# Performance work log

Hardware: AMD Instinct MI355X
Metric: run time of the kernel (lower is better)

## Reference

```python
import jax, jax.numpy as jnp
import numpy as np

B, DM, H, M, K = 2, 256, 4, 4096, 16
DIM = DM // H  # per-head feature dim = 64


def _proj(x, W, b):
    # 1x1 Conv2d on channels-first (B, C, M, K): pointwise linear over channels
    return jnp.einsum('oi,bimk->bomk', W, x) + b[None, :, None, None]


def setup_inputs() -> dict:
    rng = jax.random.key(0)
    ks = jax.random.split(rng, 11)
    s = 1.0 / np.sqrt(DM)
    return {
        'query': jax.random.normal(ks[0], (B, DM, M, 1), jnp.float32),
        'key':   jax.random.normal(ks[1], (B, DM, M, K), jnp.float32),
        'value': jax.random.normal(ks[2], (B, DM, M, K), jnp.float32),
        'Wq': jax.random.normal(ks[3], (DM, DM), jnp.float32) * s,
        'bq': jax.random.normal(ks[4], (DM,), jnp.float32) * 0.01,
        'Wk': jax.random.normal(ks[5], (DM, DM), jnp.float32) * s,
        'bk': jax.random.normal(ks[6], (DM,), jnp.float32) * 0.01,
        'Wv': jax.random.normal(ks[7], (DM, DM), jnp.float32) * s,
        'bv': jax.random.normal(ks[8], (DM,), jnp.float32) * 0.01,
        'Wm': jax.random.normal(ks[9], (DM, DM), jnp.float32) * s,
        'bm': jax.random.normal(ks[10], (DM,), jnp.float32) * 0.01,
    }


def reference(query, key, value, Wq, bq, Wk, bk, Wv, bv, Wm, bm):
    # project; torch view(B, dim, heads, -1) on channels-first => channel c -> (d=c//H, h=c%H)
    q = _proj(query, Wq, bq).reshape(B, DIM, H, M)          # (b, d, h, m)
    k = _proj(key,   Wk, bk).reshape(B, DIM, H, M, K)        # (b, d, h, m, k)
    v = _proj(value, Wv, bv).reshape(B, DIM, H, M, K)
    scores = jnp.einsum('bfhm,bfhmk->bhmk', q, k) / np.sqrt(DIM).astype(np.float32)
    prob = jax.nn.softmax(scores, axis=-1)                   # softmax over kn neighbors
    x = jnp.einsum('bhmk,bdhmk->bdhm', prob, v)              # (b, d, h, m)
    out = _proj(x.reshape(B, DM, M, 1), Wm, bm)              # merge 1x1 conv
    prob_sum = jnp.sum(prob, axis=1)                         # (b, m, k)
    return out, prob_sum
```

## Files before the change

### kernel.cpp

```cpp
#include <hip/hip_runtime.h>
#include <stdint.h>

#define DM_ 256
#define H_ 4
#define M_ 4096
#define KN_ 16
#define B_ 2
#define MK_ (M_*KN_)

typedef __attribute__((ext_vector_type(8))) short short8;
typedef __attribute__((ext_vector_type(4))) float f32x4;
typedef __attribute__((ext_vector_type(4))) unsigned short u16x4;

static __device__ __forceinline__ unsigned short f2bf(float x) {
  union { float f; uint32_t u; } v; v.f = x;
  uint32_t u = v.u + (0x7FFFu + ((v.u >> 16) & 1u));
  return (unsigned short)(u >> 16);
}
static __device__ __forceinline__ float bf2f(unsigned short x) {
  union { uint32_t u; float f; } v; v.u = ((uint32_t)x) << 16; return v.f;
}

static __device__ __forceinline__ int swz512(int col, int kbyte) {
  int f = ((col >> 2) & 7) ^ ((col & 1) << 2);
  return (col << 9) + (kbyte ^ (f << 4));
}

__global__ void prep2(const float* __restrict__ Wq, const float* __restrict__ bq,
                      const float* __restrict__ Wk, const float* __restrict__ Wv,
                      const float* __restrict__ bv, const float* __restrict__ Wm,
                      const float* __restrict__ bm,
                      unsigned short* __restrict__ W2T, unsigned short* __restrict__ Wmv,
                      float* __restrict__ qb2, float* __restrict__ btot) {
  int t = blockIdx.x * 512 + threadIdx.x;
  if (t < 262144) {
    int j = t & 7, lane = (t >> 3) & 63, rowblk = (t >> 9) & 63, kstep = t >> 15;
    int row = rowblk * 16 + (lane & 15);
    int k = kstep * 32 + (lane >> 4) * 8 + j;
    int h = row >> 8, c = row & 255;
    float v = 0.f;
#pragma unroll 8
    for (int d = 0; d < 64; ++d) v += Wq[(4 * d + h) * 256 + k] * Wk[(4 * d + h) * 256 + c];
    W2T[t] = f2bf(v);
  } else if (t < 524288) {
    int e = t - 262144;
    int j = e & 7, lane = (e >> 3) & 63, rowblk = (e >> 9) & 15, kstep = e >> 13;
    int o = rowblk * 16 + (lane & 15);
    int kidx = kstep * 32 + (lane >> 4) * 8 + j;
    int c = kidx >> 2, h = kidx & 3;
    float v = 0.f;
#pragma unroll 8
    for (int d = 0; d < 64; ++d) v += Wm[o * 256 + 4 * d + h] * Wv[(4 * d + h) * 256 + c];
    Wmv[e] = f2bf(v);
  } else if (t < 525312) {
    int r = t - 524288; int h = r >> 8, c = r & 255;
    float v = 0.f;
#pragma unroll 8
    for (int d = 0; d < 64; ++d) v += bq[4 * d + h] * Wk[(4 * d + h) * 256 + c];
    qb2[r] = v;
  } else if (t < 525568) {
    int o = t - 525312;
    float v = bm[o];
#pragma unroll 8
    for (int c2 = 0; c2 < 256; ++c2) v += Wm[o * 256 + c2] * bv[c2];
    btot[o] = v;
  }
}

__global__ __launch_bounds__(512)
void qw_gemm(const float* __restrict__ query, const unsigned short* __restrict__ W2T,
             const float* __restrict__ qb2, unsigned short* __restrict__ qWbuf) {
  __shared__ unsigned short Xl[32 * 256];
  const int tid = threadIdx.x;
  const int lane = tid & 63, wid = tid >> 6;
  const int wr = wid >> 1, wc = wid & 1;
  const int mt = blockIdx.x & 127;
  const int rt = (blockIdx.x >> 7) & 3;
  const int b = blockIdx.x >> 9;
  const int m0 = mt * 32;
  const float* Xb = query + (size_t)b * DM_ * M_ + m0;
  const int c4 = 4 * (tid & 7);
  const int ch0 = 4 * (tid >> 3);
  float4 f[4];
#pragma unroll
  for (int i = 0; i < 4; ++i) f[i] = *(const float4*)(Xb + (size_t)(ch0 + i) * M_ + c4);
#pragma unroll
  for (int j = 0; j < 4; ++j) {
    u16x4 u = { f2bf(((const float*)&f[0])[j]), f2bf(((const float*)&f[1])[j]),
                f2bf(((const float*)&f[2])[j]), f2bf(((const float*)&f[3])[j]) };
    *(u16x4*)((char*)Xl + swz512(c4 + j, 2 * ch0)) = u;
  }
  __syncthreads();
  f32x4 acc[4] = {};
  const int bcol = wc * 16 + (lane & 15);
  const int rdk = 16 * (lane >> 4);
  short8 a_cur[4], a_nxt[4];
#pragma unroll
  for (int fi = 0; fi < 4; ++fi)
    a_cur[fi] = *(const short8*)(W2T + (size_t)(((0 * 64 + rt * 16 + wr * 4 + fi) * 64 + lane) * 8));
#pragma unroll
  for (int kgs = 0; kgs < 8; ++kgs) {
    if (kgs < 7) {
#pragma unroll
      for (int fi = 0; fi < 4; ++fi)
        a_nxt[fi] = *(const short8*)(W2T + (size_t)((((kgs + 1) * 64 + rt * 16 + wr * 4 + fi) * 64 + lane) * 8));
    }
    short8 bb = *(const short8*)((const char*)Xl + swz512(bcol, 64 * kgs + rdk));
#pragma unroll
    for (int fi = 0; fi < 4; ++fi)
      acc[fi] = __builtin_amdgcn_mfma_f32_16x16x32_bf16(a_cur[fi], bb, acc[fi], 0, 0, 0);
#pragma unroll
    for (int fi = 0; fi < 4; ++fi) a_cur[fi] = a_nxt[fi];
  }
#pragma unroll
  for (int fi = 0; fi < 4; ++fi) {
#pragma unroll
    for (int r = 0; r < 4; ++r) {
      const int rr = rt * 256 + wr * 64 + fi * 16 + (lane >> 4) * 4 + r;
      qWbuf[(size_t)(b * 1024 + rr) * M_ + m0 + bcol] = f2bf(acc[fi][r] + qb2[rr]);
    }
  }
}

__global__ __launch_bounds__(512, 4)
void attn_stream(const float* __restrict__ key, const float* __restrict__ value,
                 const unsigned short* __restrict__ qWbuf,
                 unsigned short* __restrict__ pvbuf, float* __restrict__ psum) {
  __shared__ float shA[256 * 32];
  __shared__ float scx[8][4][128];
  __shared__ float prob_lds[4][8][16];
  const int tid = threadIdx.x;
  const int lane = tid & 63, w = tid >> 6;
  const int vb = (blockIdx.x & 7) * 128 + (blockIdx.x >> 3);
  const int b = vb >> 9;
  const int m0 = (vb & 511) * 8;
  const int cb = w * 32;
  const int chalf = lane >> 5;
  const int colb = m0 * KN_ + 4 * (lane & 31);
  const int mloc = (lane & 31) >> 2;
  const int kk0 = 4 * (lane & 3);
  const int r0 = tid * 2;
  uint4 qw0 = *(const uint4*)(qWbuf + (size_t)(b * 1024 + r0) * M_ + m0);
  uint4 qw1 = *(const uint4*)(qWbuf + (size_t)(b * 1024 + r0 + 1) * M_ + m0);
  __builtin_amdgcn_sched_barrier(0);
  const float* kp0 = key + (size_t)b * DM_ * MK_ + (size_t)(cb + chalf) * MK_ + colb;
  const float* vp0 = value + (size_t)b * DM_ * MK_ + (size_t)(cb + chalf) * MK_ + colb;
  f32x4 K[16];
#pragma unroll
  for (int i = 0; i < 16; ++i) K[i] = *(const f32x4*)(kp0 + (size_t)(2 * i) * MK_);
  __builtin_amdgcn_sched_barrier(0);
#pragma unroll
  for (int p = 0; p < 2; ++p) {
    const int r = r0 + p;
    const int h = r >> 8, c = r & 255;
    const uint32_t* vu = p ? (const uint32_t*)&qw1 : (const uint32_t*)&qw0;
#pragma unroll
    for (int m = 0; m < 8; ++m)
      shA[c * 32 + m * 4 + h] = bf2f((unsigned short)(vu[m >> 1] >> ((m & 1) * 16)));
  }
  __syncthreads();
  f32x4 s4[4] = {};
  f32x4 V[16];
  const int qb0 = (cb + chalf) * 32 + mloc * 4;
#pragma unroll
  for (int i = 0; i < 16; ++i) {
    V[i] = *(const f32x4*)(vp0 + (size_t)(2 * i) * MK_);
    const f32x4 qv = *(const f32x4*)&shA[qb0 + i * 64];
#pragma unroll
    for (int h = 0; h < 4; ++h) s4[h] += K[i] * qv[h];
    __builtin_amdgcn_sched_barrier(0);
  }
#pragma unroll
  for (int h = 0; h < 4; ++h)
#pragma unroll
    for (int j = 0; j < 4; ++j) {
      float v = s4[h][j];
      v += __shfl_xor(v, 32);
      s4[h][j] = v;
    }
  if (lane < 32) {
#pragma unroll
    for (int h = 0; h < 4; ++h) *(f32x4*)&scx[w][h][4 * lane] = s4[h];
  }
  __syncthreads();
  {
    const int h2 = tid >> 7, col = tid & 127;
    float sc = 0.f;
#pragma unroll
    for (int w2 = 0; w2 < 8; ++w2) sc += scx[w2][h2][col];
    sc *= 0.125f;
    float mx = sc;
#pragma unroll
    for (int d2 = 1; d2 < 16; d2 <<= 1) mx = fmaxf(mx, __shfl_xor(mx, d2));
    const float e = __expf(sc - mx);
    float sm = e;
#pragma unroll
    for (int d2 = 1; d2 < 16; d2 <<= 1) sm += __shfl_xor(sm, d2);
    prob_lds[h2][col >> 4][col & 15] = e / sm;
  }
  __syncthreads();
  if (tid < 128) {
    const int m = tid >> 4, kk = tid & 15;
    psum[(size_t)(b * M_ + m0 + m) * KN_ + kk] =
        prob_lds[0][m][kk] + prob_lds[1][m][kk] + prob_lds[2][m][kk] + prob_lds[3][m][kk];
  }
  f32x4 pr[4];
#pragma unroll
  for (int h = 0; h < 4; ++h) pr[h] = *(const f32x4*)&prob_lds[h][mloc][kk0];
#pragma unroll
  for (int j = 0; j < 16; ++j) {
    const f32x4 vv = V[j];
    float pp[4];
#pragma unroll
    for (int h = 0; h < 4; ++h)
      pp[h] = fmaf(pr[h][0], vv[0], fmaf(pr[h][1], vv[1], fmaf(pr[h][2], vv[2], pr[h][3] * vv[3])));
#pragma unroll
    for (int h = 0; h < 4; ++h) {
      pp[h] += __shfl_xor(pp[h], 1);
      pp[h] += __shfl_xor(pp[h], 2);
    }
    if ((lane & 3) == 0) {
      const int c = cb + 2 * j + chalf;
      f32x4 o = {pp[0], pp[1], pp[2], pp[3]};
      *(f32x4*)&shA[c * 32 + mloc * 4] = o;
    }
  }
  __syncthreads();
  {
    unsigned short o16[16];
#pragma unroll
    for (int ci = 0; ci < 4; ++ci) {
      f32x4 v = *(const f32x4*)&shA[(lane * 4 + ci) * 32 + w * 4];
#pragma unroll
      for (int h = 0; h < 4; ++h) o16[ci * 4 + h] = f2bf(v[h]);
    }
    unsigned short* dst = pvbuf + ((size_t)(b * M_ + m0 + w) * 1024 + lane * 16);
    *(uint4*)dst = *(const uint4*)&o16[0];
    *(uint4*)(dst + 8) = *(const uint4*)&o16[8];
  }
}

__global__ __launch_bounds__(512)
void out_gemm(const unsigned short* __restrict__ pvbuf, const unsigned short* __restrict__ Wmv,
              const float* __restrict__ btot, float* __restrict__ Out) {
  __shared__ unsigned short Xl[2][16 * 256];
  const int tid = threadIdx.x;
  const int lane = tid & 63, wid = tid >> 6;
  const int b = blockIdx.x >> 8;
  const int m0 = (blockIdx.x & 255) * 16;
  const int scol = tid & 15, sq = tid >> 4;
  const int bcol = lane & 15;
  const int rdk = 16 * (lane >> 4);
  f32x4 acc[2] = {};
  for (int kp = 0; kp < 4; ++kp) {
    {
      const unsigned short* src = pvbuf + ((size_t)(b * M_ + m0 + scol) * 1024 + kp * 256 + sq * 8);
      uint4 v0 = *(const uint4*)src;
      *(uint4*)((char*)Xl[kp & 1] + swz512(scol, sq * 16)) = v0;
    }
    __syncthreads();
    short8 a_cur[2], a_nxt[2];
#pragma unroll
    for (int fi = 0; fi < 2; ++fi)
      a_cur[fi] = *(const short8*)(Wmv + (size_t)((((kp * 8) * 16 + wid * 2 + fi) * 64 + lane) * 8));
#pragma unroll
    for (int kgs = 0; kgs < 8; ++kgs) {
      if (kgs < 7) {
#pragma unroll
        for (int fi = 0; fi < 2; ++fi)
          a_nxt[fi] = *(const short8*)(Wmv + (size_t)((((kp * 8 + kgs + 1) * 16 + wid * 2 + fi) * 64 + lane) * 8));
      }
      short8 bb = *(const short8*)((const char*)Xl[kp & 1] + swz512(bcol, 64 * kgs + rdk));
#pragma unroll
      for (int fi = 0; fi < 2; ++fi)
        acc[fi] = __builtin_amdgcn_mfma_f32_16x16x32_bf16(a_cur[fi], bb, acc[fi], 0, 0, 0);
#pragma unroll
      for (int fi = 0; fi < 2; ++fi) a_cur[fi] = a_nxt[fi];
    }
    if (kp < 3) __syncthreads();
  }
#pragma unroll
  for (int fi = 0; fi < 2; ++fi) {
#pragma unroll
    for (int r = 0; r < 4; ++r) {
      const int o = (wid * 2 + fi) * 16 + (lane >> 4) * 4 + r;
      Out[(size_t)(b * DM_ + o) * M_ + m0 + bcol] = acc[fi][r] + btot[o];
    }
  }
}

extern "C" void kernel_launch(void* const* d_in, const int* in_sizes, int n_in,
                              void* d_out, int out_size, void* d_ws, size_t ws_size,
                              hipStream_t stream) {
  const float* query = (const float*)d_in[0];
  const float* key   = (const float*)d_in[1];
  const float* value = (const float*)d_in[2];
  const float* Wq = (const float*)d_in[3];
  const float* bq = (const float*)d_in[4];
  const float* Wk = (const float*)d_in[5];
  const float* bk = (const float*)d_in[6];  (void)bk;
  const float* Wv = (const float*)d_in[7];
  const float* bv = (const float*)d_in[8];
  const float* Wm = (const float*)d_in[9];
  const float* bm = (const float*)d_in[10];
  float* out  = (float*)d_out;
  float* psum = out + (size_t)B_ * DM_ * M_;

  const size_t Wmv_off  = 524288;
  const size_t qb2_off  = 1048576;
  const size_t btot_off = 1052672;
  const size_t qW_off   = 1053696;
  const size_t pv_off   = qW_off + (size_t)B_ * 1024 * M_ * 2;

  unsigned short* W2T   = (unsigned short*)d_ws;
  unsigned short* Wmv   = (unsigned short*)((char*)d_ws + Wmv_off);
  float* qb2            = (float*)((char*)d_ws + qb2_off);
  float* btot           = (float*)((char*)d_ws + btot_off);
  unsigned short* qWbuf = (unsigned short*)((char*)d_ws + qW_off);
  unsigned short* pvbuf = (unsigned short*)((char*)d_ws + pv_off);

  prep2<<<dim3(1027), dim3(512), 0, stream>>>(Wq, bq, Wk, Wv, bv, Wm, bm, W2T, Wmv, qb2, btot);
  qw_gemm<<<dim3(B_ * 4 * 128), dim3(512), 0, stream>>>(query, W2T, qb2, qWbuf);
  attn_stream<<<dim3(B_ * (M_ / 8)), dim3(512), 0, stream>>>(key, value, qWbuf, pvbuf, psum);
  out_gemm<<<dim3(B_ * 256), dim3(512), 0, stream>>>(pvbuf, Wmv, btot, out);
}
```

Before: 117.3 us.

## Restructure attention stream kernel with smaller tiles, inline-asm loads and staged waits

The attention kernel now processes 4 queries per block instead of 8, doubling the grid, and issues all key and value loads up front via inline global_load_dwordx4. Per-step s_waitcnt counters let score and PV compute overlap the remaining in-flight loads. The qW buffer is written by qw_gemm in a per-tile interleaved layout, so one coalesced load and a bf16 LDS tile replace the old fp32 scatter. PV results are packed to bf16 in LDS before a single vector store. This aims to raise memory-level parallelism on the key/value stream, at the cost of fragile hand-counted vmcnt values and a lower occupancy hint.

```diff
diff --git a/kernel.cpp b/kernel.cpp
--- a/kernel.cpp
+++ b/kernel.cpp
@@ -17,8 +17,8 @@
   uint32_t u = v.u + (0x7FFFu + ((v.u >> 16) & 1u));
   return (unsigned short)(u >> 16);
 }
-static __device__ __forceinline__ float bf2f(unsigned short x) {
-  union { uint32_t u; float f; } v; v.u = ((uint32_t)x) << 16; return v.f;
+static __device__ __forceinline__ float u2f(uint32_t u) {
+  union { uint32_t u; float f; } v; v.u = u; return v.f;
 }
 
 static __device__ __forceinline__ int swz512(int col, int kbyte) {
@@ -74,9 +74,10 @@
   const int tid = threadIdx.x;
   const int lane = tid & 63, wid = tid >> 6;
   const int wr = wid >> 1, wc = wid & 1;
-  const int mt = blockIdx.x & 127;
-  const int rt = (blockIdx.x >> 7) & 3;
-  const int b = blockIdx.x >> 9;
+  const int vb = (blockIdx.x & 7) * 128 + (blockIdx.x >> 3);
+  const int rt = vb & 3;
+  const int mt = (vb >> 2) & 127;
+  const int b = vb >> 9;
   const int m0 = mt * 32;
   const float* Xb = query + (size_t)b * DM_ * M_ + m0;
   const int c4 = 4 * (tid & 7);
@@ -97,7 +98,7 @@
   short8 a_cur[4], a_nxt[4];
 #pragma unroll
   for (int fi = 0; fi < 4; ++fi)
-    a_cur[fi] = *(const short8*)(W2T + (size_t)(((0 * 64 + rt * 16 + wr * 4 + fi) * 64 + lane) * 8));
+    a_cur[fi] = *(const short8*)(W2T + (size_t)(((rt * 16 + wr * 4 + fi) * 64 + lane) * 8));
 #pragma unroll
   for (int kgs = 0; kgs < 8; ++kgs) {
     if (kgs < 7) {
@@ -112,79 +113,88 @@
 #pragma unroll
     for (int fi = 0; fi < 4; ++fi) a_cur[fi] = a_nxt[fi];
   }
+  const int m = m0 + bcol;
+  const int mt4 = m >> 2, mq = m & 3;
 #pragma unroll
   for (int fi = 0; fi < 4; ++fi) {
 #pragma unroll
     for (int r = 0; r < 4; ++r) {
-      const int rr = rt * 256 + wr * 64 + fi * 16 + (lane >> 4) * 4 + r;
-      qWbuf[(size_t)(b * 1024 + rr) * M_ + m0 + bcol] = f2bf(acc[fi][r] + qb2[rr]);
-    }
-  }
-}
-
-__global__ __launch_bounds__(512, 4)
+      const int c = wr * 64 + fi * 16 + (lane >> 4) * 4 + r;
+      const int rr = rt * 256 + c;
+      qWbuf[((size_t)(b * 1024 + mt4)) * 4096 + c * 16 + mq * 4 + rt] =
+          f2bf(acc[fi][r] + qb2[rr]);
+    }
+  }
+}
+
+__global__ __launch_bounds__(512, 3)
 void attn_stream(const float* __restrict__ key, const float* __restrict__ value,
                  const unsigned short* __restrict__ qWbuf,
                  unsigned short* __restrict__ pvbuf, float* __restrict__ psum) {
-  __shared__ float shA[256 * 32];
-  __shared__ float scx[8][4][128];
-  __shared__ float prob_lds[4][8][16];
+  __shared__ unsigned short qwtile[4096];
+  __shared__ float scx[8][4][64];
+  __shared__ float prob_lds[4][4][16];
   const int tid = threadIdx.x;
   const int lane = tid & 63, w = tid >> 6;
-  const int vb = (blockIdx.x & 7) * 128 + (blockIdx.x >> 3);
-  const int b = vb >> 9;
-  const int m0 = (vb & 511) * 8;
+  const int vb = (blockIdx.x & 7) * 256 + (blockIdx.x >> 3);
+  const int b = vb >> 10;
+  const int m0 = (vb & 1023) * 4;
+  const int g = lane >> 4, l15 = lane & 15;
+  const int mq = l15 & 3;
+  const int kq = 4 * (l15 >> 2);
+  const int colw = mq * 16 + kq;
   const int cb = w * 32;
-  const int chalf = lane >> 5;
-  const int colb = m0 * KN_ + 4 * (lane & 31);
-  const int mloc = (lane & 31) >> 2;
-  const int kk0 = 4 * (lane & 3);
-  const int r0 = tid * 2;
-  uint4 qw0 = *(const uint4*)(qWbuf + (size_t)(b * 1024 + r0) * M_ + m0);
-  uint4 qw1 = *(const uint4*)(qWbuf + (size_t)(b * 1024 + r0 + 1) * M_ + m0);
+  const float* kb  = key   + (size_t)b * DM_ * MK_;
+  const float* vbp = value + (size_t)b * DM_ * MK_;
+  const unsigned short* qwsrc = qWbuf + ((size_t)(b * 1024 + (m0 >> 2))) * 4096;
+  const uint32_t qwoff = (uint32_t)tid * 16u;
+  const uint32_t kvo = ((uint32_t)(cb + g) * (uint32_t)MK_ +
+                        (uint32_t)(m0 * KN_) + (uint32_t)colw) * 4u;
+  uint4 qwv;
+  f32x4 K[8], V[8];
+  asm volatile("global_load_dwordx4 %0, %1, %2" : "=v"(qwv) : "v"(qwoff), "s"(qwsrc));
+#define GK(i) asm volatile("global_load_dwordx4 %0, %1, %2" : "=v"(K[i]) : "v"(kvo + (i)*1048576u), "s"(kb))
+#define GV(i) asm volatile("global_load_dwordx4 %0, %1, %2" : "=v"(V[i]) : "v"(kvo + (i)*1048576u), "s"(vbp))
+  GK(0); GK(1); GK(2); GK(3); GK(4); GK(5); GK(6); GK(7);
+  GV(0); GV(1); GV(2); GV(3); GV(4); GV(5); GV(6); GV(7);
+#undef GK
+#undef GV
+  asm volatile("s_waitcnt vmcnt(16)" ::: "memory");
   __builtin_amdgcn_sched_barrier(0);
-  const float* kp0 = key + (size_t)b * DM_ * MK_ + (size_t)(cb + chalf) * MK_ + colb;
-  const float* vp0 = value + (size_t)b * DM_ * MK_ + (size_t)(cb + chalf) * MK_ + colb;
-  f32x4 K[16];
-#pragma unroll
-  for (int i = 0; i < 16; ++i) K[i] = *(const f32x4*)(kp0 + (size_t)(2 * i) * MK_);
-  __builtin_amdgcn_sched_barrier(0);
-#pragma unroll
-  for (int p = 0; p < 2; ++p) {
-    const int r = r0 + p;
-    const int h = r >> 8, c = r & 255;
-    const uint32_t* vu = p ? (const uint32_t*)&qw1 : (const uint32_t*)&qw0;
-#pragma unroll
-    for (int m = 0; m < 8; ++m)
-      shA[c * 32 + m * 4 + h] = bf2f((unsigned short)(vu[m >> 1] >> ((m & 1) * 16)));
-  }
-  __syncthreads();
+  *(uint4*)(qwtile + tid * 8) = qwv;
+  __syncthreads();
+  uint2 qvr[8];
+#pragma unroll
+  for (int i = 0; i < 8; ++i)
+    qvr[i] = *(const uint2*)(qwtile + ((cb + 4 * i + g) * 16 + mq * 4));
   f32x4 s4[4] = {};
-  f32x4 V[16];
-  const int qb0 = (cb + chalf) * 32 + mloc * 4;
-#pragma unroll
-  for (int i = 0; i < 16; ++i) {
-    V[i] = *(const f32x4*)(vp0 + (size_t)(2 * i) * MK_);
-    const f32x4 qv = *(const f32x4*)&shA[qb0 + i * 64];
-#pragma unroll
-    for (int h = 0; h < 4; ++h) s4[h] += K[i] * qv[h];
-    __builtin_amdgcn_sched_barrier(0);
-  }
-#pragma unroll
-  for (int h = 0; h < 4; ++h)
+#define KSTEP(i, n) do { \
+    asm volatile("s_waitcnt vmcnt(" #n ")" ::: "memory"); \
+    __builtin_amdgcn_sched_barrier(0); \
+    const uint32_t qx = qvr[i].x, qy = qvr[i].y; \
+    s4[0] += K[i] * u2f(qx << 16); s4[1] += K[i] * u2f(qx & 0xFFFF0000u); \
+    s4[2] += K[i] * u2f(qy << 16); s4[3] += K[i] * u2f(qy & 0xFFFF0000u); \
+  } while (0)
+  KSTEP(0, 15); KSTEP(1, 14); KSTEP(2, 13); KSTEP(3, 12);
+  KSTEP(4, 11); KSTEP(5, 10); KSTEP(6, 9);  KSTEP(7, 8);
+#undef KSTEP
+#pragma unroll
+  for (int h = 0; h < 4; ++h) {
 #pragma unroll
     for (int j = 0; j < 4; ++j) {
       float v = s4[h][j];
+      v += __shfl_xor(v, 16);
       v += __shfl_xor(v, 32);
       s4[h][j] = v;
     }
-  if (lane < 32) {
-#pragma unroll
-    for (int h = 0; h < 4; ++h) *(f32x4*)&scx[w][h][4 * lane] = s4[h];
-  }
-  __syncthreads();
-  {
-    const int h2 = tid >> 7, col = tid & 127;
+  }
+  if (g == 0) {
+#pragma unroll
+    for (int h = 0; h < 4; ++h) *(f32x4*)&scx[w][h][colw] = s4[h];
+  }
+  __syncthreads();
+  if (tid < 256) {
+    const int h2 = tid >> 6, col = tid & 63;
     float sc = 0.f;
 #pragma unroll
     for (int w2 = 0; w2 < 8; ++w2) sc += scx[w2][h2][col];
@@ -199,44 +209,39 @@
     prob_lds[h2][col >> 4][col & 15] = e / sm;
   }
   __syncthreads();
-  if (tid < 128) {
+  if (tid < 64) {
     const int m = tid >> 4, kk = tid & 15;
-    psum[(size_t)(b * M_ + m0 + m) * KN_ + kk] =
+    psum[((size_t)b * M_ + m0 + m) * KN_ + kk] =
         prob_lds[0][m][kk] + prob_lds[1][m][kk] + prob_lds[2][m][kk] + prob_lds[3][m][kk];
   }
   f32x4 pr[4];
 #pragma unroll
-  for (int h = 0; h < 4; ++h) pr[h] = *(const f32x4*)&prob_lds[h][mloc][kk0];
-#pragma unroll
-  for (int j = 0; j < 16; ++j) {
-    const f32x4 vv = V[j];
-    float pp[4];
-#pragma unroll
-    for (int h = 0; h < 4; ++h)
-      pp[h] = fmaf(pr[h][0], vv[0], fmaf(pr[h][1], vv[1], fmaf(pr[h][2], vv[2], pr[h][3] * vv[3])));
-#pragma unroll
-    for (int h = 0; h < 4; ++h) {
-      pp[h] += __shfl_xor(pp[h], 1);
-      pp[h] += __shfl_xor(pp[h], 2);
-    }
-    if ((lane & 3) == 0) {
-      const int c = cb + 2 * j + chalf;
-      f32x4 o = {pp[0], pp[1], pp[2], pp[3]};
-      *(f32x4*)&shA[c * 32 + mloc * 4] = o;
-    }
-  }
+  for (int h = 0; h < 4; ++h) pr[h] = *(const f32x4*)&prob_lds[h][mq][kq];
+#define PSTEP(j, n) do { \
+    asm volatile("s_waitcnt vmcnt(" #n ")" ::: "memory"); \
+    __builtin_amdgcn_sched_barrier(0); \
+    float p0 = pr[0][0]*V[j][0] + pr[0][1]*V[j][1] + pr[0][2]*V[j][2] + pr[0][3]*V[j][3]; \
+    float p1 = pr[1][0]*V[j][0] + pr[1][1]*V[j][1] + pr[1][2]*V[j][2] + pr[1][3]*V[j][3]; \
+    float p2 = pr[2][0]*V[j][0] + pr[2][1]*V[j][1] + pr[2][2]*V[j][2] + pr[2][3]*V[j][3]; \
+    float p3 = pr[3][0]*V[j][0] + pr[3][1]*V[j][1] + pr[3][2]*V[j][2] + pr[3][3]*V[j][3]; \
+    p0 += __shfl_xor(p0, 4); p0 += __shfl_xor(p0, 8); \
+    p1 += __shfl_xor(p1, 4); p1 += __shfl_xor(p1, 8); \
+    p2 += __shfl_xor(p2, 4); p2 += __shfl_xor(p2, 8); \
+    p3 += __shfl_xor(p3, 4); p3 += __shfl_xor(p3, 8); \
+    if (l15 < 4) { \
+      uint2 o; \
+      o.x = (uint32_t)f2bf(p0) | ((uint32_t)f2bf(p1) << 16); \
+      o.y = (uint32_t)f2bf(p2) | ((uint32_t)f2bf(p3) << 16); \
+      *(uint2*)(qwtile + (mq * 1024 + (cb + 4 * (j) + g) * 4)) = o; \
+    } \
+  } while (0)
+  PSTEP(0, 7); PSTEP(1, 6); PSTEP(2, 5); PSTEP(3, 4);
+  PSTEP(4, 3); PSTEP(5, 2); PSTEP(6, 1); PSTEP(7, 0);
+#undef PSTEP
   __syncthreads();
   {
-    unsigned short o16[16];
-#pragma unroll
-    for (int ci = 0; ci < 4; ++ci) {
-      f32x4 v = *(const f32x4*)&shA[(lane * 4 + ci) * 32 + w * 4];
-#pragma unroll
-      for (int h = 0; h < 4; ++h) o16[ci * 4 + h] = f2bf(v[h]);
-    }
-    unsigned short* dst = pvbuf + ((size_t)(b * M_ + m0 + w) * 1024 + lane * 16);
-    *(uint4*)dst = *(const uint4*)&o16[0];
-    *(uint4*)(dst + 8) = *(const uint4*)&o16[8];
+    uint4 ov = *(const uint4*)(qwtile + tid * 8);
+    *(uint4*)(pvbuf + (((size_t)b * M_ + m0 + (tid >> 7)) * 1024 + (tid & 127) * 8)) = ov;
   }
 }
 
@@ -321,6 +326,6 @@
 
   prep2<<<dim3(1027), dim3(512), 0, stream>>>(Wq, bq, Wk, Wv, bv, Wm, bm, W2T, Wmv, qb2, btot);
   qw_gemm<<<dim3(B_ * 4 * 128), dim3(512), 0, stream>>>(query, W2T, qb2, qWbuf);
-  attn_stream<<<dim3(B_ * (M_ / 8)), dim3(512), 0, stream>>>(key, value, qWbuf, pvbuf, psum);
+  attn_stream<<<dim3(B_ * (M_ / 4)), dim3(512), 0, stream>>>(key, value, qWbuf, pvbuf, psum);
   out_gemm<<<dim3(B_ * 256), dim3(512), 0, stream>>>(pvbuf, Wmv, btot, out);
 }
```

Result: slower. 130.6 us (+11.3%).

## Split fused attention into score, softmax and PV kernels with asm-pipelined loads

Applied to the files above, without the earlier changes.

Replaces the single attention kernel with three kernels. The first computes partial scores per channel group, the second reduces them and applies softmax while writing bf16 probabilities and psum, and the third applies the probabilities to value. The key and value streams are read with inline-asm global loads kept twelve deep, each followed by an explicit vmcnt wait, to hold many requests in flight. The cost is extra intermediate traffic through workspace buffers (partial scores and probabilities), two more launches, and workspace aliasing: prob reuses qWbuf and pvbuf reuses psbuf.

```diff
diff --git a/kernel.cpp b/kernel.cpp
--- a/kernel.cpp
+++ b/kernel.cpp
@@ -17,8 +17,8 @@
   uint32_t u = v.u + (0x7FFFu + ((v.u >> 16) & 1u));
   return (unsigned short)(u >> 16);
 }
-static __device__ __forceinline__ float bf2f(unsigned short x) {
-  union { uint32_t u; float f; } v; v.u = ((uint32_t)x) << 16; return v.f;
+static __device__ __forceinline__ float u2f(uint32_t u) {
+  union { uint32_t u; float f; } v; v.u = u; return v.f;
 }
 
 static __device__ __forceinline__ int swz512(int col, int kbyte) {
@@ -97,7 +97,7 @@
   short8 a_cur[4], a_nxt[4];
 #pragma unroll
   for (int fi = 0; fi < 4; ++fi)
-    a_cur[fi] = *(const short8*)(W2T + (size_t)(((0 * 64 + rt * 16 + wr * 4 + fi) * 64 + lane) * 8));
+    a_cur[fi] = *(const short8*)(W2T + (size_t)(((rt * 16 + wr * 4 + fi) * 64 + lane) * 8));
 #pragma unroll
   for (int kgs = 0; kgs < 8; ++kgs) {
     if (kgs < 7) {
@@ -123,120 +123,177 @@
 }
 
 __global__ __launch_bounds__(512, 4)
-void attn_stream(const float* __restrict__ key, const float* __restrict__ value,
-                 const unsigned short* __restrict__ qWbuf,
-                 unsigned short* __restrict__ pvbuf, float* __restrict__ psum) {
-  __shared__ float shA[256 * 32];
-  __shared__ float scx[8][4][128];
-  __shared__ float prob_lds[4][8][16];
+void score_part(const float* __restrict__ key, const unsigned short* __restrict__ qW,
+                float* __restrict__ psbuf) {
+  __shared__ unsigned short qsl[32 * 128 * 4];
   const int tid = threadIdx.x;
-  const int lane = tid & 63, w = tid >> 6;
-  const int vb = (blockIdx.x & 7) * 128 + (blockIdx.x >> 3);
-  const int b = vb >> 9;
-  const int m0 = (vb & 511) * 8;
-  const int cb = w * 32;
-  const int chalf = lane >> 5;
-  const int colb = m0 * KN_ + 4 * (lane & 31);
-  const int mloc = (lane & 31) >> 2;
-  const int kk0 = 4 * (lane & 3);
-  const int r0 = tid * 2;
-  uint4 qw0 = *(const uint4*)(qWbuf + (size_t)(b * 1024 + r0) * M_ + m0);
-  uint4 qw1 = *(const uint4*)(qWbuf + (size_t)(b * 1024 + r0 + 1) * M_ + m0);
+  const int bid = blockIdx.x;
+  const int cg = bid & 7, msb = (bid >> 3) & 31, b = bid >> 8;
+  const int m0 = msb * 128, C0 = cg * 32;
+  {
+    const int row = tid >> 2, part = tid & 3;
+    const int h = row >> 5, c = row & 31;
+    const unsigned short* src = qW + (size_t)(b * 1024 + h * 256 + C0 + c) * M_ + m0 + part * 32;
+#pragma unroll
+    for (int p = 0; p < 4; ++p) {
+      uint4 v = *(const uint4*)(src + p * 8);
+      const uint32_t* vu = (const uint32_t*)&v;
+#pragma unroll
+      for (int e = 0; e < 4; ++e) {
+        const int mm = part * 32 + p * 8 + e * 2;
+        qsl[(c * 128 + mm) * 4 + h]     = (unsigned short)(vu[e] & 0xffffu);
+        qsl[(c * 128 + mm + 1) * 4 + h] = (unsigned short)(vu[e] >> 16);
+      }
+    }
+  }
+  __syncthreads();
+  const int mq = tid >> 2;
+  const int kq = (tid & 3) * 4;
+  const float* kp = key + (size_t)(b * 256 + C0) * 65536 + (size_t)m0 * 16;
+  const uint32_t voff = (uint32_t)((mq * 16 + kq) * 4);
+  f32x4 K[12];
+#define GK(s, cc) asm volatile("global_load_dwordx4 %0, %1, %2" : "=v"(K[s]) : "v"(voff), "s"(kp + (size_t)(cc) * 65536))
+  GK(0,0); GK(1,1); GK(2,2); GK(3,3); GK(4,4); GK(5,5);
+  GK(6,6); GK(7,7); GK(8,8); GK(9,9); GK(10,10); GK(11,11);
+  f32x4 ps0 = {}, ps1 = {}, ps2 = {}, ps3 = {};
+#define AIT(c, n) { \
+    asm volatile("s_waitcnt vmcnt(" #n ")" ::: "memory"); \
+    __builtin_amdgcn_sched_barrier(0); \
+    uint2 qv = *(const uint2*)&qsl[((c) * 128 + mq) * 4]; \
+    float h0 = u2f(qv.x << 16), h1 = u2f(qv.x & 0xffff0000u); \
+    float h2 = u2f(qv.y << 16), h3 = u2f(qv.y & 0xffff0000u); \
+    ps0 += K[(c) % 12] * h0; ps1 += K[(c) % 12] * h1; \
+    ps2 += K[(c) % 12] * h2; ps3 += K[(c) % 12] * h3; \
+    if ((c) < 20) { GK((c) % 12, (c) + 12); } \
+  }
+  AIT(0,11) AIT(1,11) AIT(2,11) AIT(3,11) AIT(4,11) AIT(5,11) AIT(6,11) AIT(7,11)
+  AIT(8,11) AIT(9,11) AIT(10,11) AIT(11,11) AIT(12,11) AIT(13,11) AIT(14,11) AIT(15,11)
+  AIT(16,11) AIT(17,11) AIT(18,11) AIT(19,11) AIT(20,11) AIT(21,10) AIT(22,9) AIT(23,8)
+  AIT(24,7) AIT(25,6) AIT(26,5) AIT(27,4) AIT(28,3) AIT(29,2) AIT(30,1) AIT(31,0)
+#undef AIT
+#undef GK
+  float* pso = psbuf + ((size_t)((b * 8 + cg) * 4096 + m0 + mq) * 16 + kq) * 4;
+#pragma unroll
+  for (int j = 0; j < 4; ++j) {
+    f32x4 o = {ps0[j], ps1[j], ps2[j], ps3[j]};
+    *(f32x4*)(pso + j * 4) = o;
+  }
+}
+
+__global__ __launch_bounds__(512)
+void softmax_k(const float* __restrict__ psbuf, unsigned short* __restrict__ prob,
+               float* __restrict__ psum) {
+  const int tid = threadIdx.x, bid = blockIdx.x;
+  const int b = bid >> 7;
+  const int m = (bid & 127) * 32 + (tid >> 4);
+  const int cp = (tid >> 2) & 3, h = tid & 3;
+  float s[16];
+#pragma unroll
+  for (int kk = 0; kk < 16; ++kk) s[kk] = 0.f;
+#pragma unroll
+  for (int gi = 0; gi < 2; ++gi) {
+    const int g = cp * 2 + gi;
+    const float* pp = psbuf + (size_t)((b * 8 + g) * 4096 + m) * 64 + h;
+#pragma unroll
+    for (int kk = 0; kk < 16; ++kk) s[kk] += pp[kk * 4];
+  }
+#pragma unroll
+  for (int kk = 0; kk < 16; ++kk) {
+    s[kk] += __shfl_xor(s[kk], 4);
+    s[kk] += __shfl_xor(s[kk], 8);
+    s[kk] *= 0.125f;
+  }
+  float mx = s[0];
+#pragma unroll
+  for (int kk = 1; kk < 16; ++kk) mx = fmaxf(mx, s[kk]);
+  float sm = 0.f;
+#pragma unroll
+  for (int kk = 0; kk < 16; ++kk) { s[kk] = __expf(s[kk] - mx); sm += s[kk]; }
+  const float inv = 1.f / sm;
+#pragma unroll
+  for (int kk = 0; kk < 16; ++kk) s[kk] *= inv;
+  if (cp == 0) {
+    unsigned short o16[16];
+#pragma unroll
+    for (int kk = 0; kk < 16; ++kk) o16[kk] = f2bf(s[kk]);
+    unsigned short* dst = prob + ((size_t)(b * 4096 + m) * 4 + h) * 16;
+    *(uint4*)dst = *(const uint4*)&o16[0];
+    *(uint4*)(dst + 8) = *(const uint4*)&o16[8];
+  }
+#pragma unroll
+  for (int kk = 0; kk < 16; ++kk) {
+    s[kk] += __shfl_xor(s[kk], 1);
+    s[kk] += __shfl_xor(s[kk], 2);
+  }
+  if (cp == 0 && h == 0) {
+    float* dst = psum + ((size_t)b * M_ + m) * 16;
+#pragma unroll
+    for (int j = 0; j < 4; ++j) {
+      f32x4 o = {s[j * 4], s[j * 4 + 1], s[j * 4 + 2], s[j * 4 + 3]};
+      *(f32x4*)(dst + j * 4) = o;
+    }
+  }
+}
+
+__global__ __launch_bounds__(512, 4)
+void pv_part(const float* __restrict__ value, const unsigned short* __restrict__ prob,
+             unsigned short* __restrict__ pvbuf) {
+  __shared__ unsigned short pvt[128 * 132];
+  const int tid = threadIdx.x;
+  const int bid = blockIdx.x;
+  const int cg = bid & 7, msb = (bid >> 3) & 31, b = bid >> 8;
+  const int m0 = msb * 128, C0 = cg * 32;
+  const int mq = tid >> 2, kq4 = tid & 3;
+  const unsigned short* pb = prob + (size_t)(b * 4096 + m0) * 64;
+  const uint32_t pvo = (uint32_t)(mq * 128 + kq4 * 8);
+  uint2 pw0, pw1, pw2, pw3;
+  asm volatile("global_load_dwordx2 %0, %1, %2"           : "=v"(pw0) : "v"(pvo), "s"(pb));
+  asm volatile("global_load_dwordx2 %0, %1, %2 offset:32" : "=v"(pw1) : "v"(pvo), "s"(pb));
+  asm volatile("global_load_dwordx2 %0, %1, %2 offset:64" : "=v"(pw2) : "v"(pvo), "s"(pb));
+  asm volatile("global_load_dwordx2 %0, %1, %2 offset:96" : "=v"(pw3) : "v"(pvo), "s"(pb));
+  const float* vp = value + (size_t)(b * 256 + C0) * 65536 + (size_t)m0 * 16;
+  const uint32_t voff = (uint32_t)((mq * 16 + kq4 * 4) * 4);
+  f32x4 V[12];
+#define GV(s, cc) asm volatile("global_load_dwordx4 %0, %1, %2" : "=v"(V[s]) : "v"(voff), "s"(vp + (size_t)(cc) * 65536))
+  GV(0,0); GV(1,1); GV(2,2); GV(3,3); GV(4,4); GV(5,5);
+  GV(6,6); GV(7,7); GV(8,8); GV(9,9); GV(10,10); GV(11,11);
+  asm volatile("s_waitcnt vmcnt(12)" ::: "memory");
   __builtin_amdgcn_sched_barrier(0);
-  const float* kp0 = key + (size_t)b * DM_ * MK_ + (size_t)(cb + chalf) * MK_ + colb;
-  const float* vp0 = value + (size_t)b * DM_ * MK_ + (size_t)(cb + chalf) * MK_ + colb;
-  f32x4 K[16];
-#pragma unroll
-  for (int i = 0; i < 16; ++i) K[i] = *(const f32x4*)(kp0 + (size_t)(2 * i) * MK_);
-  __builtin_amdgcn_sched_barrier(0);
-#pragma unroll
-  for (int p = 0; p < 2; ++p) {
-    const int r = r0 + p;
-    const int h = r >> 8, c = r & 255;
-    const uint32_t* vu = p ? (const uint32_t*)&qw1 : (const uint32_t*)&qw0;
-#pragma unroll
-    for (int m = 0; m < 8; ++m)
-      shA[c * 32 + m * 4 + h] = bf2f((unsigned short)(vu[m >> 1] >> ((m & 1) * 16)));
-  }
-  __syncthreads();
-  f32x4 s4[4] = {};
-  f32x4 V[16];
-  const int qb0 = (cb + chalf) * 32 + mloc * 4;
-#pragma unroll
-  for (int i = 0; i < 16; ++i) {
-    V[i] = *(const f32x4*)(vp0 + (size_t)(2 * i) * MK_);
-    const f32x4 qv = *(const f32x4*)&shA[qb0 + i * 64];
-#pragma unroll
-    for (int h = 0; h < 4; ++h) s4[h] += K[i] * qv[h];
-    __builtin_amdgcn_sched_barrier(0);
-  }
-#pragma unroll
-  for (int h = 0; h < 4; ++h)
-#pragma unroll
-    for (int j = 0; j < 4; ++j) {
-      float v = s4[h][j];
-      v += __shfl_xor(v, 32);
-      s4[h][j] = v;
-    }
-  if (lane < 32) {
-#pragma unroll
-    for (int h = 0; h < 4; ++h) *(f32x4*)&scx[w][h][4 * lane] = s4[h];
-  }
+  f32x4 pr0 = {u2f(pw0.x << 16), u2f(pw0.x & 0xffff0000u), u2f(pw0.y << 16), u2f(pw0.y & 0xffff0000u)};
+  f32x4 pr1 = {u2f(pw1.x << 16), u2f(pw1.x & 0xffff0000u), u2f(pw1.y << 16), u2f(pw1.y & 0xffff0000u)};
+  f32x4 pr2 = {u2f(pw2.x << 16), u2f(pw2.x & 0xffff0000u), u2f(pw2.y << 16), u2f(pw2.y & 0xffff0000u)};
+  f32x4 pr3 = {u2f(pw3.x << 16), u2f(pw3.x & 0xffff0000u), u2f(pw3.y << 16), u2f(pw3.y & 0xffff0000u)};
+  const bool k0 = (kq4 == 0), k1 = (kq4 == 1), k2 = (kq4 == 2);
+#define CIT(c, n) { \
+    asm volatile("s_waitcnt vmcnt(" #n ")" ::: "memory"); \
+    __builtin_amdgcn_sched_barrier(0); \
+    f32x4 vv = V[(c) % 12]; \
+    float p0 = vv[0]*pr0[0] + vv[1]*pr0[1] + vv[2]*pr0[2] + vv[3]*pr0[3]; \
+    float p1 = vv[0]*pr1[0] + vv[1]*pr1[1] + vv[2]*pr1[2] + vv[3]*pr1[3]; \
+    float p2 = vv[0]*pr2[0] + vv[1]*pr2[1] + vv[2]*pr2[2] + vv[3]*pr2[3]; \
+    float p3 = vv[0]*pr3[0] + vv[1]*pr3[1] + vv[2]*pr3[2] + vv[3]*pr3[3]; \
+    p0 += __shfl_xor(p0, 1); p0 += __shfl_xor(p0, 2); \
+    p1 += __shfl_xor(p1, 1); p1 += __shfl_xor(p1, 2); \
+    p2 += __shfl_xor(p2, 1); p2 += __shfl_xor(p2, 2); \
+    p3 += __shfl_xor(p3, 1); p3 += __shfl_xor(p3, 2); \
+    float psel = k0 ? p0 : (k1 ? p1 : (k2 ? p2 : p3)); \
+    pvt[mq * 132 + (c) * 4 + kq4] = f2bf(psel); \
+    if ((c) < 20) { GV((c) % 12, (c) + 12); } \
+  }
+  CIT(0,11) CIT(1,11) CIT(2,11) CIT(3,11) CIT(4,11) CIT(5,11) CIT(6,11) CIT(7,11)
+  CIT(8,11) CIT(9,11) CIT(10,11) CIT(11,11) CIT(12,11) CIT(13,11) CIT(14,11) CIT(15,11)
+  CIT(16,11) CIT(17,11) CIT(18,11) CIT(19,11) CIT(20,11) CIT(21,10) CIT(22,9) CIT(23,8)
+  CIT(24,7) CIT(25,6) CIT(26,5) CIT(27,4) CIT(28,3) CIT(29,2) CIT(30,1) CIT(31,0)
+#undef CIT
+#undef GV
   __syncthreads();
   {
-    const int h2 = tid >> 7, col = tid & 127;
-    float sc = 0.f;
-#pragma unroll
-    for (int w2 = 0; w2 < 8; ++w2) sc += scx[w2][h2][col];
-    sc *= 0.125f;
-    float mx = sc;
-#pragma unroll
-    for (int d2 = 1; d2 < 16; d2 <<= 1) mx = fmaxf(mx, __shfl_xor(mx, d2));
-    const float e = __expf(sc - mx);
-    float sm = e;
-#pragma unroll
-    for (int d2 = 1; d2 < 16; d2 <<= 1) sm += __shfl_xor(sm, d2);
-    prob_lds[h2][col >> 4][col & 15] = e / sm;
-  }
-  __syncthreads();
-  if (tid < 128) {
-    const int m = tid >> 4, kk = tid & 15;
-    psum[(size_t)(b * M_ + m0 + m) * KN_ + kk] =
-        prob_lds[0][m][kk] + prob_lds[1][m][kk] + prob_lds[2][m][kk] + prob_lds[3][m][kk];
-  }
-  f32x4 pr[4];
-#pragma unroll
-  for (int h = 0; h < 4; ++h) pr[h] = *(const f32x4*)&prob_lds[h][mloc][kk0];
-#pragma unroll
-  for (int j = 0; j < 16; ++j) {
-    const f32x4 vv = V[j];
-    float pp[4];
-#pragma unroll
-    for (int h = 0; h < 4; ++h)
-      pp[h] = fmaf(pr[h][0], vv[0], fmaf(pr[h][1], vv[1], fmaf(pr[h][2], vv[2], pr[h][3] * vv[3])));
-#pragma unroll
-    for (int h = 0; h < 4; ++h) {
-      pp[h] += __shfl_xor(pp[h], 1);
-      pp[h] += __shfl_xor(pp[h], 2);
-    }
-    if ((lane & 3) == 0) {
-      const int c = cb + 2 * j + chalf;
-      f32x4 o = {pp[0], pp[1], pp[2], pp[3]};
-      *(f32x4*)&shA[c * 32 + mloc * 4] = o;
-    }
-  }
-  __syncthreads();
-  {
-    unsigned short o16[16];
-#pragma unroll
-    for (int ci = 0; ci < 4; ++ci) {
-      f32x4 v = *(const f32x4*)&shA[(lane * 4 + ci) * 32 + w * 4];
-#pragma unroll
-      for (int h = 0; h < 4; ++h) o16[ci * 4 + h] = f2bf(v[h]);
-    }
-    unsigned short* dst = pvbuf + ((size_t)(b * M_ + m0 + w) * 1024 + lane * 16);
-    *(uint4*)dst = *(const uint4*)&o16[0];
-    *(uint4*)(dst + 8) = *(const uint4*)&o16[8];
+    const int row = tid >> 2, part = tid & 3;
+    unsigned short* dst = pvbuf + (size_t)(b * 4096 + m0 + row) * 1024 + C0 * 4 + part * 32;
+    const unsigned short* srcl = &pvt[row * 132 + part * 32];
+#pragma unroll
+    for (int j = 0; j < 4; ++j)
+      *(uint4*)(dst + j * 8) = *(const uint4*)(srcl + j * 8);
   }
 }
 
@@ -310,17 +367,21 @@
   const size_t qb2_off  = 1048576;
   const size_t btot_off = 1052672;
   const size_t qW_off   = 1053696;
-  const size_t pv_off   = qW_off + (size_t)B_ * 1024 * M_ * 2;
+  const size_t ps_off   = qW_off + (size_t)B_ * 1024 * M_ * 2;
 
   unsigned short* W2T   = (unsigned short*)d_ws;
   unsigned short* Wmv   = (unsigned short*)((char*)d_ws + Wmv_off);
   float* qb2            = (float*)((char*)d_ws + qb2_off);
   float* btot           = (float*)((char*)d_ws + btot_off);
   unsigned short* qWbuf = (unsigned short*)((char*)d_ws + qW_off);
-  unsigned short* pvbuf = (unsigned short*)((char*)d_ws + pv_off);
+  unsigned short* prob  = qWbuf;
+  float* psbuf          = (float*)((char*)d_ws + ps_off);
+  unsigned short* pvbuf = (unsigned short*)((char*)d_ws + ps_off);
 
   prep2<<<dim3(1027), dim3(512), 0, stream>>>(Wq, bq, Wk, Wv, bv, Wm, bm, W2T, Wmv, qb2, btot);
   qw_gemm<<<dim3(B_ * 4 * 128), dim3(512), 0, stream>>>(query, W2T, qb2, qWbuf);
-  attn_stream<<<dim3(B_ * (M_ / 8)), dim3(512), 0, stream>>>(key, value, qWbuf, pvbuf, psum);
+  score_part<<<dim3(512), dim3(512), 0, stream>>>(key, qWbuf, psbuf);
+  softmax_k<<<dim3(256), dim3(512), 0, stream>>>(psbuf, prob, psum);
+  pv_part<<<dim3(512), dim3(512), 0, stream>>>(value, prob, pvbuf);
   out_gemm<<<dim3(B_ * 256), dim3(512), 0, stream>>>(pvbuf, Wmv, btot, out);
 }
```

After: 407.9 us. 248% more time.

## Fuse attention streaming with output projection GEMM in one kernel

Applied to the files above, without the earlier changes.

Merges the attention-streaming kernel and the output GEMM into a single kernel. Each block now handles 16 query points instead of 8 and keeps the bf16 PV result in shared memory, so the pvbuf round trip through global memory and one launch are gone. Key/value access is reorganised so each thread reads float4 along the neighbor axis with a per-row channel split, and reductions use shuffles in place of LDS staging. The trade-offs are half as many blocks (512), which lowers parallelism for the memory-bound key/value stream, and an unpipelined MFMA loop that loads weights directly from global memory.

```diff
diff --git a/kernel.cpp b/kernel.cpp
--- a/kernel.cpp
+++ b/kernel.cpp
@@ -17,8 +17,8 @@
   uint32_t u = v.u + (0x7FFFu + ((v.u >> 16) & 1u));
   return (unsigned short)(u >> 16);
 }
-static __device__ __forceinline__ float bf2f(unsigned short x) {
-  union { uint32_t u; float f; } v; v.u = ((uint32_t)x) << 16; return v.f;
+static __device__ __forceinline__ float u2f(uint32_t u) {
+  union { uint32_t u; float f; } v; v.u = u; return v.f;
 }
 
 static __device__ __forceinline__ int swz512(int col, int kbyte) {
@@ -97,7 +97,7 @@
   short8 a_cur[4], a_nxt[4];
 #pragma unroll
   for (int fi = 0; fi < 4; ++fi)
-    a_cur[fi] = *(const short8*)(W2T + (size_t)(((0 * 64 + rt * 16 + wr * 4 + fi) * 64 + lane) * 8));
+    a_cur[fi] = *(const short8*)(W2T + (size_t)(((rt * 16 + wr * 4 + fi) * 64 + lane) * 8));
 #pragma unroll
   for (int kgs = 0; kgs < 8; ++kgs) {
     if (kgs < 7) {
@@ -123,168 +123,125 @@
 }
 
 __global__ __launch_bounds__(512, 4)
-void attn_stream(const float* __restrict__ key, const float* __restrict__ value,
-                 const unsigned short* __restrict__ qWbuf,
-                 unsigned short* __restrict__ pvbuf, float* __restrict__ psum) {
-  __shared__ float shA[256 * 32];
-  __shared__ float scx[8][4][128];
-  __shared__ float prob_lds[4][8][16];
+void fused_attn(const float* __restrict__ key, const float* __restrict__ value,
+                const unsigned short* __restrict__ qW, const unsigned short* __restrict__ Wmv,
+                const float* __restrict__ btot, float* __restrict__ out,
+                float* __restrict__ psum) {
+  __shared__ unsigned short sh[16384];
   const int tid = threadIdx.x;
-  const int lane = tid & 63, w = tid >> 6;
-  const int vb = (blockIdx.x & 7) * 128 + (blockIdx.x >> 3);
-  const int b = vb >> 9;
-  const int m0 = (vb & 511) * 8;
-  const int cb = w * 32;
-  const int chalf = lane >> 5;
-  const int colb = m0 * KN_ + 4 * (lane & 31);
-  const int mloc = (lane & 31) >> 2;
-  const int kk0 = 4 * (lane & 3);
-  const int r0 = tid * 2;
-  uint4 qw0 = *(const uint4*)(qWbuf + (size_t)(b * 1024 + r0) * M_ + m0);
-  uint4 qw1 = *(const uint4*)(qWbuf + (size_t)(b * 1024 + r0 + 1) * M_ + m0);
-  __builtin_amdgcn_sched_barrier(0);
-  const float* kp0 = key + (size_t)b * DM_ * MK_ + (size_t)(cb + chalf) * MK_ + colb;
-  const float* vp0 = value + (size_t)b * DM_ * MK_ + (size_t)(cb + chalf) * MK_ + colb;
-  f32x4 K[16];
-#pragma unroll
-  for (int i = 0; i < 16; ++i) K[i] = *(const f32x4*)(kp0 + (size_t)(2 * i) * MK_);
-  __builtin_amdgcn_sched_barrier(0);
-#pragma unroll
-  for (int p = 0; p < 2; ++p) {
-    const int r = r0 + p;
-    const int h = r >> 8, c = r & 255;
-    const uint32_t* vu = p ? (const uint32_t*)&qw1 : (const uint32_t*)&qw0;
-#pragma unroll
-    for (int m = 0; m < 8; ++m)
-      shA[c * 32 + m * 4 + h] = bf2f((unsigned short)(vu[m >> 1] >> ((m & 1) * 16)));
-  }
-  __syncthreads();
-  f32x4 s4[4] = {};
-  f32x4 V[16];
-  const int qb0 = (cb + chalf) * 32 + mloc * 4;
-#pragma unroll
-  for (int i = 0; i < 16; ++i) {
-    V[i] = *(const f32x4*)(vp0 + (size_t)(2 * i) * MK_);
-    const f32x4 qv = *(const f32x4*)&shA[qb0 + i * 64];
-#pragma unroll
-    for (int h = 0; h < 4; ++h) s4[h] += K[i] * qv[h];
-    __builtin_amdgcn_sched_barrier(0);
-  }
-#pragma unroll
-  for (int h = 0; h < 4; ++h)
-#pragma unroll
-    for (int j = 0; j < 4; ++j) {
-      float v = s4[h][j];
-      v += __shfl_xor(v, 32);
-      s4[h][j] = v;
-    }
-  if (lane < 32) {
-#pragma unroll
-    for (int h = 0; h < 4; ++h) *(f32x4*)&scx[w][h][4 * lane] = s4[h];
-  }
-  __syncthreads();
+  const int lane = tid & 63;
+  const int vb = (blockIdx.x & 7) * 64 + (blockIdx.x >> 3);
+  const int b = vb >> 8;
+  const int mt = vb & 255;
+  const int m0 = mt * 16;
   {
-    const int h2 = tid >> 7, col = tid & 127;
-    float sc = 0.f;
-#pragma unroll
-    for (int w2 = 0; w2 < 8; ++w2) sc += scx[w2][h2][col];
-    sc *= 0.125f;
-    float mx = sc;
-#pragma unroll
-    for (int d2 = 1; d2 < 16; d2 <<= 1) mx = fmaxf(mx, __shfl_xor(mx, d2));
-    const float e = __expf(sc - mx);
-    float sm = e;
-#pragma unroll
-    for (int d2 = 1; d2 < 16; d2 <<= 1) sm += __shfl_xor(sm, d2);
-    prob_lds[h2][col >> 4][col & 15] = e / sm;
-  }
-  __syncthreads();
-  if (tid < 128) {
-    const int m = tid >> 4, kk = tid & 15;
-    psum[(size_t)(b * M_ + m0 + m) * KN_ + kk] =
-        prob_lds[0][m][kk] + prob_lds[1][m][kk] + prob_lds[2][m][kk] + prob_lds[3][m][kk];
-  }
-  f32x4 pr[4];
-#pragma unroll
-  for (int h = 0; h < 4; ++h) pr[h] = *(const f32x4*)&prob_lds[h][mloc][kk0];
-#pragma unroll
-  for (int j = 0; j < 16; ++j) {
-    const f32x4 vv = V[j];
-    float pp[4];
-#pragma unroll
-    for (int h = 0; h < 4; ++h)
-      pp[h] = fmaf(pr[h][0], vv[0], fmaf(pr[h][1], vv[1], fmaf(pr[h][2], vv[2], pr[h][3] * vv[3])));
-#pragma unroll
-    for (int h = 0; h < 4; ++h) {
-      pp[h] += __shfl_xor(pp[h], 1);
-      pp[h] += __shfl_xor(pp[h], 2);
-    }
-    if ((lane & 3) == 0) {
-      const int c = cb + 2 * j + chalf;
-      f32x4 o = {pp[0], pp[1], pp[2], pp[3]};
-      *(f32x4*)&shA[c * 32 + mloc * 4] = o;
+    const int c = tid & 255, hh = (tid >> 8) << 1;
+    uint4 rv[2][2];
+#pragma unroll
+    for (int h2 = 0; h2 < 2; ++h2) {
+      const unsigned short* src = qW + ((size_t)(b * 1024 + (hh + h2) * 256 + c)) * M_ + m0;
+      rv[h2][0] = *(const uint4*)(src);
+      rv[h2][1] = *(const uint4*)(src + 8);
+    }
+    const unsigned short* rs = (const unsigned short*)rv;
+#pragma unroll
+    for (int q = 0; q < 16; ++q) {
+      const int slot = (q + c) & 15;
+      const uint32_t o = (uint32_t)rs[q] | ((uint32_t)rs[16 + q] << 16);
+      *(uint32_t*)&sh[c * 64 + slot * 4 + hh] = o;
+    }
+  }
+  __syncthreads();
+  const int mq = tid >> 5;
+  const int cs = (tid >> 2) & 7;
+  const int kq = tid & 3;
+  const float* kp = key + (size_t)(b * 256) * 65536 + (size_t)m0 * 16;
+  const float* vp = value + (size_t)(b * 256) * 65536 + (size_t)m0 * 16;
+  const int moff = mq * 16 + kq * 4;
+  f32x4 ps0 = {}, ps1 = {}, ps2 = {}, ps3 = {};
+#pragma unroll 2
+  for (int cc = 0; cc < 8; ++cc) {
+#pragma unroll
+    for (int i = 0; i < 4; ++i) {
+      const int c = cc * 32 + cs * 4 + i;
+      const f32x4 kv = *(const f32x4*)(kp + (size_t)c * 65536 + moff);
+      const int slot = (mq + c) & 15;
+      const uint2 qv = *(const uint2*)&sh[c * 64 + slot * 4];
+      ps0 += kv * u2f(qv.x << 16);
+      ps1 += kv * u2f(qv.x & 0xffff0000u);
+      ps2 += kv * u2f(qv.y << 16);
+      ps3 += kv * u2f(qv.y & 0xffff0000u);
+    }
+  }
+#pragma unroll
+  for (int j = 0; j < 4; ++j) {
+    ps0[j] += __shfl_xor(ps0[j], 4); ps0[j] += __shfl_xor(ps0[j], 8); ps0[j] += __shfl_xor(ps0[j], 16);
+    ps1[j] += __shfl_xor(ps1[j], 4); ps1[j] += __shfl_xor(ps1[j], 8); ps1[j] += __shfl_xor(ps1[j], 16);
+    ps2[j] += __shfl_xor(ps2[j], 4); ps2[j] += __shfl_xor(ps2[j], 8); ps2[j] += __shfl_xor(ps2[j], 16);
+    ps3[j] += __shfl_xor(ps3[j], 4); ps3[j] += __shfl_xor(ps3[j], 8); ps3[j] += __shfl_xor(ps3[j], 16);
+  }
+  f32x4 pr0, pr1, pr2, pr3;
+#define SOFT(ps, pr) { \
+    f32x4 s = ps * 0.125f; \
+    float mx = fmaxf(fmaxf(s[0], s[1]), fmaxf(s[2], s[3])); \
+    mx = fmaxf(mx, __shfl_xor(mx, 1)); mx = fmaxf(mx, __shfl_xor(mx, 2)); \
+    f32x4 e; \
+    e[0] = __expf(s[0] - mx); e[1] = __expf(s[1] - mx); \
+    e[2] = __expf(s[2] - mx); e[3] = __expf(s[3] - mx); \
+    float sm = e[0] + e[1] + e[2] + e[3]; \
+    sm += __shfl_xor(sm, 1); sm += __shfl_xor(sm, 2); \
+    const float inv = 1.f / sm; \
+    pr[0] = e[0] * inv; pr[1] = e[1] * inv; pr[2] = e[2] * inv; pr[3] = e[3] * inv; \
+  }
+  SOFT(ps0, pr0) SOFT(ps1, pr1) SOFT(ps2, pr2) SOFT(ps3, pr3)
+#undef SOFT
+  if (cs == 0) {
+    f32x4 pp = pr0 + pr1 + pr2 + pr3;
+    *(f32x4*)(psum + ((size_t)b * M_ + m0 + mq) * KN_ + kq * 4) = pp;
+  }
+  __syncthreads();
+#pragma unroll 2
+  for (int cc = 0; cc < 8; ++cc) {
+#pragma unroll
+    for (int i = 0; i < 4; ++i) {
+      const int c = cc * 32 + cs * 4 + i;
+      const f32x4 vv = *(const f32x4*)(vp + (size_t)c * 65536 + moff);
+      float p0 = vv[0] * pr0[0] + vv[1] * pr0[1] + vv[2] * pr0[2] + vv[3] * pr0[3];
+      float p1 = vv[0] * pr1[0] + vv[1] * pr1[1] + vv[2] * pr1[2] + vv[3] * pr1[3];
+      float p2 = vv[0] * pr2[0] + vv[1] * pr2[1] + vv[2] * pr2[2] + vv[3] * pr2[3];
+      float p3 = vv[0] * pr3[0] + vv[1] * pr3[1] + vv[2] * pr3[2] + vv[3] * pr3[3];
+      p0 += __shfl_xor(p0, 1); p0 += __shfl_xor(p0, 2);
+      p1 += __shfl_xor(p1, 1); p1 += __shfl_xor(p1, 2);
+      p2 += __shfl_xor(p2, 1); p2 += __shfl_xor(p2, 2);
+      p3 += __shfl_xor(p3, 1); p3 += __shfl_xor(p3, 2);
+      if (kq == 0) {
+        uint2 o;
+        o.x = (uint32_t)f2bf(p0) | ((uint32_t)f2bf(p1) << 16);
+        o.y = (uint32_t)f2bf(p2) | ((uint32_t)f2bf(p3) << 16);
+        *(uint2*)((char*)sh + ((mq * 2048 + c * 8) ^ ((mq & 7) << 4))) = o;
+      }
     }
   }
   __syncthreads();
   {
-    unsigned short o16[16];
-#pragma unroll
-    for (int ci = 0; ci < 4; ++ci) {
-      f32x4 v = *(const f32x4*)&shA[(lane * 4 + ci) * 32 + w * 4];
-#pragma unroll
-      for (int h = 0; h < 4; ++h) o16[ci * 4 + h] = f2bf(v[h]);
-    }
-    unsigned short* dst = pvbuf + ((size_t)(b * M_ + m0 + w) * 1024 + lane * 16);
-    *(uint4*)dst = *(const uint4*)&o16[0];
-    *(uint4*)(dst + 8) = *(const uint4*)&o16[8];
-  }
-}
-
-__global__ __launch_bounds__(512)
-void out_gemm(const unsigned short* __restrict__ pvbuf, const unsigned short* __restrict__ Wmv,
-              const float* __restrict__ btot, float* __restrict__ Out) {
-  __shared__ unsigned short Xl[2][16 * 256];
-  const int tid = threadIdx.x;
-  const int lane = tid & 63, wid = tid >> 6;
-  const int b = blockIdx.x >> 8;
-  const int m0 = (blockIdx.x & 255) * 16;
-  const int scol = tid & 15, sq = tid >> 4;
-  const int bcol = lane & 15;
-  const int rdk = 16 * (lane >> 4);
-  f32x4 acc[2] = {};
-  for (int kp = 0; kp < 4; ++kp) {
-    {
-      const unsigned short* src = pvbuf + ((size_t)(b * M_ + m0 + scol) * 1024 + kp * 256 + sq * 8);
-      uint4 v0 = *(const uint4*)src;
-      *(uint4*)((char*)Xl[kp & 1] + swz512(scol, sq * 16)) = v0;
-    }
-    __syncthreads();
-    short8 a_cur[2], a_nxt[2];
-#pragma unroll
-    for (int fi = 0; fi < 2; ++fi)
-      a_cur[fi] = *(const short8*)(Wmv + (size_t)((((kp * 8) * 16 + wid * 2 + fi) * 64 + lane) * 8));
-#pragma unroll
-    for (int kgs = 0; kgs < 8; ++kgs) {
-      if (kgs < 7) {
-#pragma unroll
-        for (int fi = 0; fi < 2; ++fi)
-          a_nxt[fi] = *(const short8*)(Wmv + (size_t)((((kp * 8 + kgs + 1) * 16 + wid * 2 + fi) * 64 + lane) * 8));
-      }
-      short8 bb = *(const short8*)((const char*)Xl[kp & 1] + swz512(bcol, 64 * kgs + rdk));
-#pragma unroll
-      for (int fi = 0; fi < 2; ++fi)
-        acc[fi] = __builtin_amdgcn_mfma_f32_16x16x32_bf16(a_cur[fi], bb, acc[fi], 0, 0, 0);
-#pragma unroll
-      for (int fi = 0; fi < 2; ++fi) a_cur[fi] = a_nxt[fi];
-    }
-    if (kp < 3) __syncthreads();
-  }
-#pragma unroll
-  for (int fi = 0; fi < 2; ++fi) {
+    const int wid = tid >> 6;
+    const int bcol = lane & 15;
+    const int kgrp = lane >> 4;
+    f32x4 acc0 = {}, acc1 = {};
+    for (int kgs = 0; kgs < 32; ++kgs) {
+      const int byte = (bcol * 2048 + kgs * 64 + kgrp * 16) ^ ((bcol & 7) << 4);
+      const short8 bb = *(const short8*)((const char*)sh + byte);
+      const short8 a0 = *(const short8*)(Wmv + (size_t)(((kgs * 16 + wid * 2 + 0) * 64 + lane) * 8));
+      const short8 a1 = *(const short8*)(Wmv + (size_t)(((kgs * 16 + wid * 2 + 1) * 64 + lane) * 8));
+      acc0 = __builtin_amdgcn_mfma_f32_16x16x32_bf16(a0, bb, acc0, 0, 0, 0);
+      acc1 = __builtin_amdgcn_mfma_f32_16x16x32_bf16(a1, bb, acc1, 0, 0, 0);
+    }
 #pragma unroll
     for (int r = 0; r < 4; ++r) {
-      const int o = (wid * 2 + fi) * 16 + (lane >> 4) * 4 + r;
-      Out[(size_t)(b * DM_ + o) * M_ + m0 + bcol] = acc[fi][r] + btot[o];
+      const int o0 = (wid * 2 + 0) * 16 + kgrp * 4 + r;
+      const int o1 = (wid * 2 + 1) * 16 + kgrp * 4 + r;
+      out[((size_t)(b * DM_ + o0)) * M_ + m0 + bcol] = acc0[r] + btot[o0];
+      out[((size_t)(b * DM_ + o1)) * M_ + m0 + bcol] = acc1[r] + btot[o1];
     }
   }
 }
@@ -310,17 +267,14 @@
   const size_t qb2_off  = 1048576;
   const size_t btot_off = 1052672;
   const size_t qW_off   = 1053696;
-  const size_t pv_off   = qW_off + (size_t)B_ * 1024 * M_ * 2;
 
   unsigned short* W2T   = (unsigned short*)d_ws;
   unsigned short* Wmv   = (unsigned short*)((char*)d_ws + Wmv_off);
   float* qb2            = (float*)((char*)d_ws + qb2_off);
   float* btot           = (float*)((char*)d_ws + btot_off);
   unsigned short* qWbuf = (unsigned short*)((char*)d_ws + qW_off);
-  unsigned short* pvbuf = (unsigned short*)((char*)d_ws + pv_off);
 
   prep2<<<dim3(1027), dim3(512), 0, stream>>>(Wq, bq, Wk, Wv, bv, Wm, bm, W2T, Wmv, qb2, btot);
   qw_gemm<<<dim3(B_ * 4 * 128), dim3(512), 0, stream>>>(query, W2T, qb2, qWbuf);
-  attn_stream<<<dim3(B_ * (M_ / 8)), dim3(512), 0, stream>>>(key, value, qWbuf, pvbuf, psum);
-  out_gemm<<<dim3(B_ * 256), dim3(512), 0, stream>>>(pvbuf, Wmv, btot, out);
-}
+  fused_attn<<<dim3(512), dim3(512), 0, stream>>>(key, value, qWbuf, Wmv, btot, out, psum);
+}
```

After: 108.1 us. -7.9%, faster.
